# Performance work log

Hardware: AMD Instinct MI355X
Metric: run time of the kernel (lower is better)

## Reference

```python
import jax, jax.numpy as jnp
import numpy as np


def _local_linear(x, W, b=None):
    # Faithful to Local_Linear: split last dim into G groups, apply per-group
    # Linear, then stack groups on the LAST axis and flatten -> output channel
    # index is o*G + g (interleaved), NOT block-diagonal order.
    B, N, C = x.shape
    G, og, ig = W.shape
    y = jnp.einsum('bngi,goi->bngo', x.reshape(B, N, G, ig), W)  # [B,N,G,og]
    if b is not None:
        y = y + b
    return jnp.swapaxes(y, -1, -2).reshape(B, N, G * og)  # [B,N,og,G] -> flat


def setup_inputs() -> dict:
    key = jax.random.key(0)
    ks = jax.random.split(key, 6)
    B, N, dim, H = 16, 8192, 128, 2
    hd = dim // H
    s = 1.0 / np.sqrt(hd).astype(np.float32)
    return {
        'x': jax.random.normal(ks[0], (B, N, dim), jnp.float32),
        'Wk': jax.random.normal(ks[1], (H, hd, hd), jnp.float32) * s,
        'Wv': jax.random.normal(ks[2], (H, hd, hd), jnp.float32) * s,
        'Wp': jax.random.normal(ks[3], (H, hd, hd), jnp.float32) * s,
        'bp': jax.random.normal(ks[4], (H, hd), jnp.float32) * 0.01,
        'mem': jax.random.normal(ks[5], (H, hd), jnp.float32) * 0.02,
    }


def reference(x, Wk, Wv, Wp, bp, mem):
    B, N, C = x.shape
    H, hd = mem.shape
    scale = hd ** -0.5
    # k, v: [B, H, N, hd] (view of interleaved grouped-linear output, as in torch)
    k = _local_linear(x, Wk).reshape(B, N, H, hd).transpose(0, 2, 1, 3)
    v = _local_linear(x, Wv).reshape(B, N, H, hd).transpose(0, 2, 1, 3)
    # The query (memory_bank) is identical for every position, so the [N,N]
    # attention matrix has identical rows -> compute one row per (b,h).
    s = jnp.einsum('hd,bhmd->bhm', mem, k) * scale          # logits over keys
    a = jax.nn.softmax(s, axis=-1)                          # [B,H,N]
    row = jnp.einsum('bhm,bhmd->bhd', a, v)                 # [B,H,hd]
    # torch does out.view(B,N,-1) WITHOUT permuting heads back; [B,H,N,hd]
    # reshaped directly to [B,N,C]. Replicate that exact layout.
    out = jnp.broadcast_to(row[:, :, None, :], (B, H, N, hd)).reshape(B, N, C)
    return _local_linear(out, Wp, bp)
```

## Files before the change

### kernel.cpp

```cpp
#include <hip/hip_runtime.h>
#include <hip/hip_bf16.h>

#define B_      16
#define N_      8192
#define C_      128
#define HD_     64
#define TILE_N  128
#define NBLK    (N_ / TILE_N)
#define PART_STRIDE 260

typedef float v4f __attribute__((ext_vector_type(4)));

__global__ __launch_bounds__(256) void k_partial(
    const float* __restrict__ x,
    const float* __restrict__ Wk,
    const float* __restrict__ mem,
    float* __restrict__ part)
{
    __shared__ float qeff0[C_], qeff1[C_];
    __shared__ float sp0[2][TILE_N], sp1[2][TILE_N];
    __shared__ float sl0[TILE_N], sl1[TILE_N];
    __shared__ float pa0[2][C_], pa1[2][C_];
    __shared__ float redm[8];

    const int t   = threadIdx.x;
    const int blk = blockIdx.x;
    const int b   = blk / NBLK;
    const int n0  = (blk % NBLK) * TILE_N;

    {
        const int h = t >> 7, c = t & 127, g = c >> 6, i = c & 63;
        const float* wkb = Wk + g * 4096 + (h * 32) * 64 + i;
        const float* mr  = mem + h * 64 + g;
        float a = 0.f;
        #pragma unroll
        for (int j = 0; j < 32; ++j) a += mr[2 * j] * wkb[j * 64];
        if (h == 0) qeff0[c] = 0.125f * a; else qeff1[c] = 0.125f * a;
    }
    __syncthreads();

    const int r = t & 127, half = t >> 7;
    {
        const float4* xr = (const float4*)(x + ((size_t)b * N_ + n0 + r) * C_ + half * 64);
        float p0 = 0.f, p1 = 0.f;
        #pragma unroll
        for (int v = 0; v < 16; ++v) {
            const float4 q = xr[v];
            const int c0 = half * 64 + v * 4;
            p0 += q.x * qeff0[c0]     + q.y * qeff0[c0 + 1]
                + q.z * qeff0[c0 + 2] + q.w * qeff0[c0 + 3];
            p1 += q.x * qeff1[c0]     + q.y * qeff1[c0 + 1]
                + q.z * qeff1[c0 + 2] + q.w * qeff1[c0 + 3];
        }
        sp0[half][r] = p0;
        sp1[half][r] = p1;
    }
    __syncthreads();

    float s0 = 0.f, s1 = 0.f;
    if (t < TILE_N) {
        s0 = sp0[0][t] + sp0[1][t];
        s1 = sp1[0][t] + sp1[1][t];
    }
    float m0 = s0, m1 = s1;
    #pragma unroll
    for (int off = 32; off > 0; off >>= 1) {
        m0 = fmaxf(m0, __shfl_xor(m0, off));
        m1 = fmaxf(m1, __shfl_xor(m1, off));
    }
    if (t == 0)  { redm[0] = m0; redm[1] = m1; }
    if (t == 64) { redm[2] = m0; redm[3] = m1; }
    __syncthreads();
    m0 = fmaxf(redm[0], redm[2]);
    m1 = fmaxf(redm[1], redm[3]);

    float w0 = 0.f, w1 = 0.f;
    if (t < TILE_N) {
        w0 = __expf(s0 - m0);
        w1 = __expf(s1 - m1);
        sl0[t] = w0;
        sl1[t] = w1;
    }
    float l0 = w0, l1 = w1;
    #pragma unroll
    for (int off = 32; off > 0; off >>= 1) {
        l0 += __shfl_xor(l0, off);
        l1 += __shfl_xor(l1, off);
    }
    if (t == 0)  { redm[4] = l0; redm[5] = l1; }
    if (t == 64) { redm[6] = l0; redm[7] = l1; }
    __syncthreads();

    {
        const int c = t & 127, rh = t >> 7;
        const float* xcol = x + ((size_t)b * N_ + n0 + rh * 64) * C_ + c;
        const float* wr0 = &sl0[rh * 64];
        const float* wr1 = &sl1[rh * 64];
        float a0 = 0.f, a1 = 0.f;
        #pragma unroll 8
        for (int k = 0; k < 64; ++k) {
            const float xf = xcol[(size_t)k * C_];
            a0 += wr0[k] * xf;
            a1 += wr1[k] * xf;
        }
        pa0[rh][c] = a0;
        pa1[rh][c] = a1;
    }
    __syncthreads();

    float* p = part + (size_t)blk * PART_STRIDE;
    if (t < C_) {
        p[4 + t]       = pa0[0][t] + pa0[1][t];
        p[4 + C_ + t]  = pa1[0][t] + pa1[1][t];
    }
    if (t == 0) {
        p[0] = m0; p[1] = m1;
        p[2] = redm[4] + redm[6];
        p[3] = redm[5] + redm[7];
    }
}

__global__ __launch_bounds__(256) void k_combine(
    const float* __restrict__ part,
    const float* __restrict__ Wv,
    const float* __restrict__ Wp,
    const float* __restrict__ bp,
    float* __restrict__ Fbuf)
{
    __shared__ float ml[4][NBLK];
    __shared__ float xan[2][C_];
    __shared__ float rowv[2][HD_];

    const int t = threadIdx.x;
    const int b = blockIdx.x;

    if (t < NBLK) {
        const float* p = part + ((size_t)b * NBLK + t) * PART_STRIDE;
        ml[0][t] = p[0]; ml[1][t] = p[1]; ml[2][t] = p[2]; ml[3][t] = p[3];
    }
    __syncthreads();

    const int h = t >> 7, c = t & 127;
    float M = -1e30f;
    for (int k = 0; k < NBLK; ++k) M = fmaxf(M, ml[h][k]);
    float L = 0.f;
    for (int k = 0; k < NBLK; ++k) L += ml[2 + h][k] * __expf(ml[h][k] - M);
    float xa = 0.f;
    for (int k = 0; k < NBLK; ++k) {
        const float* p = part + ((size_t)b * NBLK + k) * PART_STRIDE;
        xa += p[4 + h * C_ + c] * __expf(ml[h][k] - M);
    }
    xan[h][c] = xa / L;
    __syncthreads();

    if (t < 128) {
        const int hh = t >> 6, d = t & 63, g = d & 1, o = hh * 32 + (d >> 1);
        const float* wv = Wv + g * 4096 + o * 64;
        const float* xv = &xan[hh][g * 64];
        float acc = 0.f;
        for (int i = 0; i < 64; ++i) acc += xv[i] * wv[i];
        rowv[hh][d] = acc;
    }
    __syncthreads();

    {
        const int hh = t >> 7, cc = t & 127, g = cc & 1, o = cc >> 1;
        const float* wp = Wp + g * 4096 + o * 64;
        float acc = bp[g * 64 + o];
        for (int i = 0; i < 64; ++i) acc += rowv[hh][i] * wp[i];
        Fbuf[(b * 2 + hh) * C_ + cc] = acc;
    }
}

__global__ __launch_bounds__(256) void k_bcast(
    const v4f* __restrict__ F4,
    v4f* __restrict__ out4)
{
    __shared__ v4f Ftab[1024];
    const int t = threadIdx.x;
    for (int i = t; i < 1024; i += 256) Ftab[i] = F4[i];
    __syncthreads();

    size_t idx = (size_t)blockIdx.x * 256 + t;
    const size_t stride = (size_t)2048 * 256;
    #pragma unroll
    for (int k = 0; k < 8; ++k) {
        const v4f v = Ftab[((idx >> 17) << 5) | (idx & 31)];
        __builtin_nontemporal_store(v, &out4[idx]);
        idx += stride;
    }
}

extern "C" void kernel_launch(void* const* d_in, const int* in_sizes, int n_in,
                              void* d_out, int out_size, void* d_ws, size_t ws_size,
                              hipStream_t stream)
{
    const float* x   = (const float*)d_in[0];
    const float* Wk  = (const float*)d_in[1];
    const float* Wv  = (const float*)d_in[2];
    const float* Wp  = (const float*)d_in[3];
    const float* bp  = (const float*)d_in[4];
    const float* mem = (const float*)d_in[5];

    float* part = (float*)d_ws;
    float* Fbuf = (float*)((char*)d_ws + (size_t)B_ * NBLK * PART_STRIDE * sizeof(float));

    k_partial<<<dim3(B_ * NBLK), dim3(256), 0, stream>>>(x, Wk, mem, part);
    k_combine<<<dim3(B_), dim3(256), 0, stream>>>(part, Wv, Wp, bp, Fbuf);
    k_bcast<<<dim3(2048), dim3(256), 0, stream>>>((const v4f*)Fbuf,
                                                  (v4f*)d_out);
}
```

Baseline: 143.1 us.

## Fuse combine and broadcast into one kernel with redundant per-block combine

Replaces the 16-block combine kernel and the separate broadcast kernel with one 1024-block kernel. Each block redoes the softmax merge and the two small matvecs for its batch and head, then writes its own 128-row output tile directly. This drops a kernel launch and the global round trip through Fbuf, and spreads the combine across many blocks instead of only 16. In exchange the combine arithmetic is repeated 32 times per head, which adds redundant reads of the partials.

```diff
diff --git a/kernel.cpp b/kernel.cpp
--- a/kernel.cpp
+++ b/kernel.cpp
@@ -120,75 +120,82 @@
     }
 }
 
-__global__ __launch_bounds__(256) void k_combine(
+__global__ __launch_bounds__(256) void k_fused(
     const float* __restrict__ part,
     const float* __restrict__ Wv,
     const float* __restrict__ Wp,
     const float* __restrict__ bp,
-    float* __restrict__ Fbuf)
+    v4f* __restrict__ out4)
 {
-    __shared__ float ml[4][NBLK];
-    __shared__ float xan[2][C_];
-    __shared__ float rowv[2][HD_];
-
-    const int t = threadIdx.x;
-    const int b = blockIdx.x;
+    __shared__ float msh[NBLK], lsh[NBLK], wsh[NBLK];
+    __shared__ float pa[2][C_];
+    __shared__ float xan[C_];
+    __shared__ float rowv[HD_];
+    __shared__ float Ff[C_];
+
+    const int t   = threadIdx.x;
+    const int blk = blockIdx.x;
+    const int b   = blk >> 6;
+    const int tl  = blk & 63;
+    const int h   = tl >> 5;
+
+    const float* pb = part + (size_t)b * NBLK * PART_STRIDE;
 
     if (t < NBLK) {
-        const float* p = part + ((size_t)b * NBLK + t) * PART_STRIDE;
-        ml[0][t] = p[0]; ml[1][t] = p[1]; ml[2][t] = p[2]; ml[3][t] = p[3];
-    }
-    __syncthreads();
-
-    const int h = t >> 7, c = t & 127;
+        const float* p = pb + t * PART_STRIDE;
+        msh[t] = p[h];
+        lsh[t] = p[2 + h];
+    }
+    __syncthreads();
+
     float M = -1e30f;
-    for (int k = 0; k < NBLK; ++k) M = fmaxf(M, ml[h][k]);
+    #pragma unroll
+    for (int k = 0; k < NBLK; ++k) M = fmaxf(M, msh[k]);
     float L = 0.f;
-    for (int k = 0; k < NBLK; ++k) L += ml[2 + h][k] * __expf(ml[h][k] - M);
-    float xa = 0.f;
-    for (int k = 0; k < NBLK; ++k) {
-        const float* p = part + ((size_t)b * NBLK + k) * PART_STRIDE;
-        xa += p[4 + h * C_ + c] * __expf(ml[h][k] - M);
-    }
-    xan[h][c] = xa / L;
-    __syncthreads();
-
-    if (t < 128) {
-        const int hh = t >> 6, d = t & 63, g = d & 1, o = hh * 32 + (d >> 1);
+    #pragma unroll
+    for (int k = 0; k < NBLK; ++k) L += lsh[k] * __expf(msh[k] - M);
+    if (t < NBLK) wsh[t] = __expf(msh[t] - M);
+    __syncthreads();
+
+    {
+        const int c = t & 127, kh = t >> 7;
+        const float* q  = pb + (size_t)(kh * 32) * PART_STRIDE + 4 + h * C_ + c;
+        const float* wr = &wsh[kh * 32];
+        float a = 0.f;
+        #pragma unroll 8
+        for (int k = 0; k < 32; ++k) a += wr[k] * q[(size_t)k * PART_STRIDE];
+        pa[kh][c] = a;
+    }
+    __syncthreads();
+    if (t < C_) xan[t] = (pa[0][t] + pa[1][t]) / L;
+    __syncthreads();
+
+    if (t < HD_) {
+        const int g = t & 1, o = h * 32 + (t >> 1);
         const float* wv = Wv + g * 4096 + o * 64;
-        const float* xv = &xan[hh][g * 64];
+        const float* xv = &xan[g * 64];
         float acc = 0.f;
+        #pragma unroll 8
         for (int i = 0; i < 64; ++i) acc += xv[i] * wv[i];
-        rowv[hh][d] = acc;
-    }
-    __syncthreads();
-
-    {
-        const int hh = t >> 7, cc = t & 127, g = cc & 1, o = cc >> 1;
+        rowv[t] = acc;
+    }
+    __syncthreads();
+
+    if (t < C_) {
+        const int g = t & 1, o = t >> 1;
         const float* wp = Wp + g * 4096 + o * 64;
         float acc = bp[g * 64 + o];
-        for (int i = 0; i < 64; ++i) acc += rowv[hh][i] * wp[i];
-        Fbuf[(b * 2 + hh) * C_ + cc] = acc;
-    }
-}
-
-__global__ __launch_bounds__(256) void k_bcast(
-    const v4f* __restrict__ F4,
-    v4f* __restrict__ out4)
-{
-    __shared__ v4f Ftab[1024];
-    const int t = threadIdx.x;
-    for (int i = t; i < 1024; i += 256) Ftab[i] = F4[i];
-    __syncthreads();
-
-    size_t idx = (size_t)blockIdx.x * 256 + t;
-    const size_t stride = (size_t)2048 * 256;
-    #pragma unroll
-    for (int k = 0; k < 8; ++k) {
-        const v4f v = Ftab[((idx >> 17) << 5) | (idx & 31)];
-        __builtin_nontemporal_store(v, &out4[idx]);
-        idx += stride;
-    }
+        #pragma unroll 8
+        for (int i = 0; i < 64; ++i) acc += rowv[i] * wp[i];
+        Ff[t] = acc;
+    }
+    __syncthreads();
+
+    const v4f val = *(const v4f*)&Ff[(t & 31) * 4];
+    v4f* dst = out4 + (size_t)b * (N_ * (C_ / 4)) + (size_t)tl * (TILE_N * (C_ / 4)) + t;
+    #pragma unroll
+    for (int k = 0; k < 16; ++k)
+        __builtin_nontemporal_store(val, dst + k * 256);
 }
 
 extern "C" void kernel_launch(void* const* d_in, const int* in_sizes, int n_in,
@@ -203,10 +210,8 @@
     const float* mem = (const float*)d_in[5];
 
     float* part = (float*)d_ws;
-    float* Fbuf = (float*)((char*)d_ws + (size_t)B_ * NBLK * PART_STRIDE * sizeof(float));
 
     k_partial<<<dim3(B_ * NBLK), dim3(256), 0, stream>>>(x, Wk, mem, part);
-    k_combine<<<dim3(B_), dim3(256), 0, stream>>>(part, Wv, Wp, bp, Fbuf);
-    k_bcast<<<dim3(2048), dim3(256), 0, stream>>>((const v4f*)Fbuf,
-                                                  (v4f*)d_out);
+    k_fused<<<dim3(B_ * NBLK), dim3(256), 0, stream>>>(part, Wv, Wp, bp,
+                                                       (v4f*)d_out);
 }
```

New measurement: 139.6 us. 1.03x faster.
